# Kernel tuning notes

Measured on AMD Instinct MI355X. Metric: run time of the kernel, lower is better.

Reference implementation:

```python
import math
import jax, jax.numpy as jnp
import numpy as np

B, S, T, C, H = 4, 100, 128, 256, 256
NH, DH = 4, 32            # num_attention_heads//2, hidden_size//num_attention_heads
AH = NH * DH              # all_head_size = 128
FH = 32                   # fire_hidden_size
MAX_SP, MAX_TM, MAX_DOY = 180.0, 365.0, 182.0


def _fire(dist, c, w1, w2, max_dist):
    # FIREDistanceBias: log-compressed distance -> MLP(1->FH, SiLU, FH->1, no bias)
    c = jnp.maximum(c, 0.0)
    d = jnp.log(c * dist + 1.0) / jnp.log(c * max_dist + 1.0)
    h = jax.nn.silu(d[..., None] * w1[:, 0])   # (..., FH)
    return h @ w2[0]                            # (...,)


def setup_inputs() -> dict:
    key = jax.random.key(0)
    ks = jax.random.split(key, 20)
    p = 0.02
    inp = {
        "hidden_states": jax.random.normal(ks[0], (B, S, T, H), jnp.float32),
        "source_embeddings": jax.random.normal(ks[1], (B, S, C, H), jnp.float32),
        "attention_mask": jnp.zeros((B, 1, 1, T, C), jnp.float32),
        "st_dist": jax.random.uniform(ks[2], (B, T, C, 2), jnp.float32)
                   * jnp.array([MAX_SP, MAX_TM], jnp.float32),
        "st_doy_dist": jax.random.uniform(ks[3], (B, T, C), jnp.float32) * MAX_DOY,
        # attention projections (Linear H->AH with bias), output dense (AH->H)
        "Wq": jax.random.normal(ks[4], (AH, H), jnp.float32) * p,
        "bq": jnp.zeros((AH,), jnp.float32),
        "Wk": jax.random.normal(ks[5], (AH, H), jnp.float32) * p,
        "bk": jnp.zeros((AH,), jnp.float32),
        "Wv": jax.random.normal(ks[6], (AH, H), jnp.float32) * p,
        "bv": jnp.zeros((AH,), jnp.float32),
        "Wo": jax.random.normal(ks[7], (H, AH), jnp.float32) * p,
        "bo": jnp.zeros((H,), jnp.float32),
        # FIRE params: spatial / temporal / seasonal
        "c_s": jnp.float32(100.0),
        "w1_s": jax.random.normal(ks[8], (FH, 1), jnp.float32) * 0.5,
        "w2_s": jax.random.normal(ks[9], (1, FH), jnp.float32) * 0.5,
        "c_t": jnp.float32(100.0),
        "w1_t": jax.random.normal(ks[10], (FH, 1), jnp.float32) * 0.5,
        "w2_t": jax.random.normal(ks[11], (1, FH), jnp.float32) * 0.5,
        "c_d": jnp.float32(100.0),
        "w1_d": jax.random.normal(ks[12], (FH, 1), jnp.float32) * 0.5,
        "w2_d": jax.random.normal(ks[13], (1, FH), jnp.float32) * 0.5,
        # per-species log scales (init zeros in torch)
        "s_log_scale": jnp.zeros((S,), jnp.float32),
        "t_log_scale": jnp.zeros((S,), jnp.float32),
    }
    return inp


def reference(hidden_states, source_embeddings, attention_mask, st_dist, st_doy_dist,
              Wq, bq, Wk, bk, Wv, bv, Wo, bo,
              c_s, w1_s, w2_s, c_t, w1_t, w2_t, c_d, w1_d, w2_d,
              s_log_scale, t_log_scale):
    # FIRE distance biases over (B, T, C)
    sb = _fire(st_dist[..., 0], c_s, w1_s, w2_s, MAX_SP)
    tb = _fire(st_dist[..., 1], c_t, w1_t, w2_t, MAX_TM)
    db = _fire(st_doy_dist, c_d, w1_d, w2_d, MAX_DOY)
    # (B, S, T, C): species-scaled spatial+temporal + seasonal bias
    bias = (sb[:, None] * jnp.exp(s_log_scale)[None, :, None, None]
            + tb[:, None] * jnp.exp(t_log_scale)[None, :, None, None]
            + db[:, None])

    # projections; split heads: (B,S,L,AH) -> (B,S,NH,L,DH)
    q = (hidden_states @ Wq.T + bq).reshape(B, S, T, NH, DH).transpose(0, 1, 3, 2, 4)
    k = (source_embeddings @ Wk.T + bk).reshape(B, S, C, NH, DH).transpose(0, 1, 3, 2, 4)
    v = (source_embeddings @ Wv.T + bv).reshape(B, S, C, NH, DH).transpose(0, 1, 3, 2, 4)

    scores = jnp.einsum('bshtd,bshcd->bshtc', q, k) / math.sqrt(DH)
    scores = scores + attention_mask + bias[:, :, None]   # mask (B,1,1,T,C), bias (B,S,1,T,C)
    probs = jax.nn.softmax(scores, axis=-1)
    ctx = jnp.einsum('bshtc,bshcd->bshtd', probs, v)
    ctx = ctx.transpose(0, 1, 3, 2, 4).reshape(B, S, T, AH)
    return ctx @ Wo.T + bo   # STCrossOutput dense (dropout=0, eval)
```

## Files before the change

### kernel.cpp

```cpp
#include <hip/hip_runtime.h>
#include <hip/hip_bf16.h>
#include <math.h>

#define Bdim 4
#define Sdim 100
#define Tdim 128
#define Cdim 256
#define Hdim 256
#define NHd  4
#define DHd  32
#define AHd  128

typedef short bf16x8 __attribute__((ext_vector_type(8)));
typedef float f32x4 __attribute__((ext_vector_type(4)));

#define WAITCNT_V(n) do { \
  asm volatile("s_waitcnt vmcnt(" #n ")" ::: "memory"); \
  __builtin_amdgcn_sched_barrier(0); \
} while (0)

__device__ __forceinline__ short f2b(float x) {
  unsigned u = __float_as_uint(x);
  unsigned r = (u + 0x7FFF + ((u >> 16) & 1)) >> 16;
  return (short)r;
}

__device__ __forceinline__ void split2(float x, short& hi, short& lo) {
  unsigned u = __float_as_uint(x) & 0xFFFF0000u;
  hi = (short)(u >> 16);
  lo = f2b(x - __uint_as_float(u));
}

__device__ __forceinline__ float fire_eval(float dist, float c,
                                           const float* __restrict__ w1,
                                           const float* __restrict__ w2,
                                           float maxd) {
  c = fmaxf(c, 0.0f);
  float d = logf(fmaf(c, dist, 1.0f)) / logf(fmaf(c, maxd, 1.0f));
  float acc = 0.0f;
#pragma unroll
  for (int j = 0; j < 32; ++j) {
    float x = d * w1[j];
    float h = x / (1.0f + expf(-x));
    acc = fmaf(h, w2[j], acc);
  }
  return acc;
}

__global__ __launch_bounds__(256) void fire_bias_kernel(
    const float* __restrict__ st_dist, const float* __restrict__ st_doy,
    const float* __restrict__ mask,
    const float* __restrict__ c_s, const float* __restrict__ w1_s, const float* __restrict__ w2_s,
    const float* __restrict__ c_t, const float* __restrict__ w1_t, const float* __restrict__ w2_t,
    const float* __restrict__ c_d, const float* __restrict__ w1_d, const float* __restrict__ w2_d,
    float* __restrict__ sbF, float* __restrict__ tbF, float* __restrict__ dbF) {
  int i = blockIdx.x * 256 + threadIdx.x;
  if (i >= Bdim * Tdim * Cdim) return;
  int c = i & (Cdim - 1);
  int t = (i >> 8) & (Tdim - 1);
  int b = i >> 15;
  float2 dv = ((const float2*)st_dist)[i];
  float sv = fire_eval(dv.x, c_s[0], w1_s, w2_s, 180.0f);
  float tv = fire_eval(dv.y, c_t[0], w1_t, w2_t, 365.0f);
  float db = fire_eval(st_doy[i], c_d[0], w1_d, w2_d, 182.0f) + mask[i];
  int wt = t >> 4, lg = (t & 15) >> 2, r = t & 3;
  int nt = c >> 4, lr = c & 15;
  size_t off = ((((size_t)(b * 8 + wt) * 16 + nt) * 64) + lg * 16 + lr) * 4 + r;
  sbF[off] = sv;
  tbF[off] = tv;
  dbF[off] = db;
}

__global__ __launch_bounds__(256) void wsplit_pack(
    const float* __restrict__ Wq, const float* __restrict__ Wk,
    const float* __restrict__ Wv, const float* __restrict__ Wo,
    short* __restrict__ pack) {
  int which = blockIdx.y;
  const float* W = which == 0 ? Wq : which == 1 ? Wk : which == 2 ? Wv : Wo;
  int idx = blockIdx.x * 256 + threadIdx.x;
  int j = idx & 7;
  int l = (idx >> 3) & 63;
  int frag = idx >> 9;
  int nt, kk8, Kd;
  if (which == 3) { nt = frag & 15; kk8 = frag >> 4; Kd = 128; }
  else           { nt = frag & 7;  kk8 = frag >> 3; Kd = 256; }
  int n = nt * 16 + (l & 15);
  int k = kk8 * 32 + (l >> 4) * 8 + j;
  float val = W[(size_t)n * Kd + k];
  short h, lo_;
  if (which == 3) split2(val, h, lo_);
  else { h = f2b(val); lo_ = 0; }
  pack[(size_t)which * 65536 + idx] = h;
  pack[(size_t)which * 65536 + 32768 + idx] = lo_;
}

__global__ __launch_bounds__(256, 2) void phase1(
    const float* __restrict__ se,
    const short* __restrict__ Wkp, const float* __restrict__ bk,
    const short* __restrict__ Wvp, const float* __restrict__ bv,
    short* __restrict__ Ko, short* __restrict__ Vo,
    const float* __restrict__ hs, const short* __restrict__ Wqp,
    const float* __restrict__ bq, short* __restrict__ Qb, float scale) {
  __shared__ short wlds[2][16 * 512];
  const int bid = blockIdx.x;
  const int tid = threadIdx.x;
  const int l = tid & 63, w = tid >> 6;
  const int lr = l & 15, lg = l >> 4;
  const int g = bid / 3, m = bid - g * 3;

  if (m < 2) {
    const int m0 = (g * 2 + m) * 128;
    const float* ap0 = se + (size_t)(m0 + w * 32 + lr) * 256 + lg * 8;
    const float* ap1 = ap0 + (size_t)16 * 256;

    auto stage = [&](int buf, int kk) {
#pragma unroll
      for (int r = 0; r < 4; ++r) {
        int f = w + 4 * r;
        const short* gsrc = ((f >> 3) ? Wvp : Wkp) + ((size_t)(kk * 8 + (f & 7)) * 64 + l) * 8;
        int loff = __builtin_amdgcn_readfirstlane(buf * 8192 + f * 512);
        __builtin_amdgcn_global_load_lds(gsrc, &wlds[0][0] + loff, 16, 0, 0);
      }
    };

    f32x4 accK[2][8] = {}, accV[2][8] = {};
    stage(0, 0);
    float4 c0a = *(const float4*)ap0;
    float4 c0b = *(const float4*)(ap0 + 4);
    float4 c1a = *(const float4*)ap1;
    float4 c1b = *(const float4*)(ap1 + 4);
#pragma unroll
    for (int kk = 0; kk < 8; ++kk) {
      const int buf = kk & 1;
      float4 n0a, n0b, n1a, n1b;
      if (kk < 7) {
        stage(buf ^ 1, kk + 1);
        const int nk = (kk + 1) * 32;
        n0a = *(const float4*)(ap0 + nk);
        n0b = *(const float4*)(ap0 + nk + 4);
        n1a = *(const float4*)(ap1 + nk);
        n1b = *(const float4*)(ap1 + nk + 4);
      }
      bf16x8 af[2];
      {
        float a0[8] = {c0a.x, c0a.y, c0a.z, c0a.w, c0b.x, c0b.y, c0b.z, c0b.w};
        float a1[8] = {c1a.x, c1a.y, c1a.z, c1a.w, c1b.x, c1b.y, c1b.z, c1b.w};
#pragma unroll
        for (int e = 0; e < 8; ++e) { af[0][e] = f2b(a0[e]); af[1][e] = f2b(a1[e]); }
      }
      if (kk < 7) { WAITCNT_V(8); } else { WAITCNT_V(0); }
      __builtin_amdgcn_s_barrier();
      const short* lb = &wlds[0][0] + buf * 8192 + l * 8;
#pragma unroll
      for (int nt = 0; nt < 8; ++nt) {
        bf16x8 kw = *(const bf16x8*)(lb + nt * 512);
        bf16x8 vw = *(const bf16x8*)(lb + (8 + nt) * 512);
#pragma unroll
        for (int mi = 0; mi < 2; ++mi) {
          accK[mi][nt] = __builtin_amdgcn_mfma_f32_16x16x32_bf16(af[mi], kw, accK[mi][nt], 0, 0, 0);
          accV[mi][nt] = __builtin_amdgcn_mfma_f32_16x16x32_bf16(af[mi], vw, accV[mi][nt], 0, 0, 0);
        }
      }
      __builtin_amdgcn_s_barrier();
      if (kk < 7) { c0a = n0a; c0b = n0b; c1a = n1a; c1b = n1b; }
    }
#pragma unroll
    for (int mi = 0; mi < 2; ++mi)
#pragma unroll
      for (int nt = 0; nt < 8; ++nt)
#pragma unroll
        for (int r = 0; r < 4; ++r) {
          size_t row = (size_t)(m0 + w * 32 + mi * 16 + lg * 4 + r) * 128 + nt * 16 + lr;
          Ko[row] = f2b(accK[mi][nt][r] + bk[nt * 16 + lr]);
          Vo[row] = f2b(accV[mi][nt][r] + bv[nt * 16 + lr]);
        }
  } else {
    const int m0 = g * 128;
    const float* ap0 = hs + (size_t)(m0 + w * 32 + lr) * 256 + lg * 8;
    const float* ap1 = ap0 + (size_t)16 * 256;

    auto stage = [&](int buf, int kk) {
#pragma unroll
      for (int r = 0; r < 2; ++r) {
        int f = w + 4 * r;
        const short* gsrc = Wqp + ((size_t)(kk * 8 + f) * 64 + l) * 8;
        int loff = __builtin_amdgcn_readfirstlane(buf * 8192 + f * 512);
        __builtin_amdgcn_global_load_lds(gsrc, &wlds[0][0] + loff, 16, 0, 0);
      }
    };

    f32x4 acc[2][8] = {};
    stage(0, 0);
    float4 c0a = *(const float4*)ap0;
    float4 c0b = *(const float4*)(ap0 + 4);
    float4 c1a = *(const float4*)ap1;
    float4 c1b = *(const float4*)(ap1 + 4);
#pragma unroll
    for (int kk = 0; kk < 8; ++kk) {
      const int buf = kk & 1;
      float4 n0a, n0b, n1a, n1b;
      if (kk < 7) {
        stage(buf ^ 1, kk + 1);
        const int nk = (kk + 1) * 32;
        n0a = *(const float4*)(ap0 + nk);
        n0b = *(const float4*)(ap0 + nk + 4);
        n1a = *(const float4*)(ap1 + nk);
        n1b = *(const float4*)(ap1 + nk + 4);
      }
      bf16x8 af[2];
      {
        float a0[8] = {c0a.x, c0a.y, c0a.z, c0a.w, c0b.x, c0b.y, c0b.z, c0b.w};
        float a1[8] = {c1a.x, c1a.y, c1a.z, c1a.w, c1b.x, c1b.y, c1b.z, c1b.w};
#pragma unroll
        for (int e = 0; e < 8; ++e) { af[0][e] = f2b(a0[e]); af[1][e] = f2b(a1[e]); }
      }
      if (kk < 7) { WAITCNT_V(6); } else { WAITCNT_V(0); }
      __builtin_amdgcn_s_barrier();
      const short* lb = &wlds[0][0] + buf * 8192 + l * 8;
#pragma unroll
      for (int nt = 0; nt < 8; ++nt) {
        bf16x8 wv = *(const bf16x8*)(lb + nt * 512);
#pragma unroll
        for (int mi = 0; mi < 2; ++mi)
          acc[mi][nt] = __builtin_amdgcn_mfma_f32_16x16x32_bf16(af[mi], wv, acc[mi][nt], 0, 0, 0);
      }
      __builtin_amdgcn_s_barrier();
      if (kk < 7) { c0a = n0a; c0b = n0b; c1a = n1a; c1b = n1b; }
    }
#pragma unroll
    for (int mi = 0; mi < 2; ++mi)
#pragma unroll
      for (int nt = 0; nt < 8; ++nt)
#pragma unroll
        for (int r = 0; r < 4; ++r)
          Qb[(size_t)(m0 + w * 32 + mi * 16 + lg * 4 + r) * 128 + nt * 16 + lr] =
              f2b((acc[mi][nt][r] + bq[nt * 16 + lr]) * scale);
  }
}

__global__ __launch_bounds__(256, 2) void proj_o_mfma(
    const short* __restrict__ Ahi, const short* __restrict__ Alo,
    const short* __restrict__ Wp, const float* __restrict__ bias,
    float* __restrict__ O) {
  __shared__ short wlds[2][32 * 512];
  const int tid = threadIdx.x;
  const int l = tid & 63, w = tid >> 6;
  const int lr = l & 15, lg = l >> 4;
  const int m0 = blockIdx.x * 128;
  const short* ah0 = Ahi + (size_t)(m0 + w * 32 + lr) * 128 + lg * 8;
  const short* al0 = Alo + (size_t)(m0 + w * 32 + lr) * 128 + lg * 8;
  const short* ah1 = ah0 + (size_t)16 * 128;
  const short* al1 = al0 + (size_t)16 * 128;

  auto stage = [&](int buf, int kk) {
#pragma unroll
    for (int r = 0; r < 8; ++r) {
      int f = w + 4 * r;
      const short* gsrc = Wp + ((f >> 4) ? 32768 : 0)
                          + ((size_t)(kk * 16 + (f & 15)) * 64 + l) * 8;
      int loff = __builtin_amdgcn_readfirstlane(buf * 16384 + f * 512);
      __builtin_amdgcn_global_load_lds(gsrc, &wlds[0][0] + loff, 16, 0, 0);
    }
  };

  f32x4 acc[2][16] = {};
  stage(0, 0);
  bf16x8 ch0 = *(const bf16x8*)ah0;
  bf16x8 cl0 = *(const bf16x8*)al0;
  bf16x8 ch1 = *(const bf16x8*)ah1;
  bf16x8 cl1 = *(const bf16x8*)al1;
#pragma unroll
  for (int kk = 0; kk < 4; ++kk) {
    const int buf = kk & 1;
    bf16x8 nh0, nl0, nh1, nl1;
    if (kk < 3) {
      stage(buf ^ 1, kk + 1);
      const int nk = (kk + 1) * 32;
      nh0 = *(const bf16x8*)(ah0 + nk);
      nl0 = *(const bf16x8*)(al0 + nk);
      nh1 = *(const bf16x8*)(ah1 + nk);
      nl1 = *(const bf16x8*)(al1 + nk);
    }
    if (kk < 3) { WAITCNT_V(12); } else { WAITCNT_V(0); }
    __builtin_amdgcn_s_barrier();
    bf16x8 ahi[2] = {ch0, ch1};
    bf16x8 alo[2] = {cl0, cl1};
    const short* lb = &wlds[0][0] + buf * 16384 + l * 8;
#pragma unroll
    for (int nt = 0; nt < 16; ++nt) {
      bf16x8 whi = *(const bf16x8*)(lb + nt * 512);
      bf16x8 wlo = *(const bf16x8*)(lb + (16 + nt) * 512);
#pragma unroll
      for (int mi = 0; mi < 2; ++mi) {
        acc[mi][nt] = __builtin_amdgcn_mfma_f32_16x16x32_bf16(ahi[mi], whi, acc[mi][nt], 0, 0, 0);
        acc[mi][nt] = __builtin_amdgcn_mfma_f32_16x16x32_bf16(ahi[mi], wlo, acc[mi][nt], 0, 0, 0);
        acc[mi][nt] = __builtin_amdgcn_mfma_f32_16x16x32_bf16(alo[mi], whi, acc[mi][nt], 0, 0, 0);
      }
    }
    __builtin_amdgcn_s_barrier();
    if (kk < 3) { ch0 = nh0; cl0 = nl0; ch1 = nh1; cl1 = nl1; }
  }
#pragma unroll
  for (int mi = 0; mi < 2; ++mi)
#pragma unroll
    for (int nt = 0; nt < 16; ++nt)
#pragma unroll
      for (int r = 0; r < 4; ++r)
        O[(size_t)(m0 + w * 32 + mi * 16 + lg * 4 + r) * 256 + nt * 16 + lr] =
            acc[mi][nt][r] + bias[nt * 16 + lr];
}

__global__ __launch_bounds__(512, 2) void attn_mfma(
    const short* __restrict__ Qb, const short* __restrict__ Kb,
    const short* __restrict__ Vb,
    const float* __restrict__ sbF, const float* __restrict__ tbF,
    const float* __restrict__ dbF,
    const float* __restrict__ sls, const float* __restrict__ tls,
    short* __restrict__ Chi, short* __restrict__ Clo) {
  __shared__ short vfrag[8][2][64][8];
  __shared__ short pbuf[8][16 * 36];

  const int tid = threadIdx.x;
  const int l = tid & 63;
  const int w = tid >> 6;
  const int lr = l & 15, lg = l >> 4;
  const int bid = blockIdx.x;
  const int xcd = bid & 7;
  const int i_  = bid >> 3;
  const int bs  = xcd * 50 + (i_ >> 2);
  const int h   = i_ & 3;
  const int s = bs % Sdim, b = bs / Sdim;
  const float es = __expf(sls[s]);
  const float et = __expf(tls[s]);

  const size_t kvbase = (size_t)bs * Cdim * AHd + h * DHd;
  const size_t qbase  = (size_t)bs * Tdim * AHd + h * DHd;

  bf16x8 qf = *(const bf16x8*)(Qb + qbase + (size_t)(w * 16 + lr) * AHd + lg * 8);
  bf16x8 kf[16];
#pragma unroll
  for (int nt = 0; nt < 16; ++nt)
    kf[nt] = *(const bf16x8*)(Kb + kvbase + (size_t)(nt * 16 + lr) * AHd + lg * 8);

#pragma unroll
  for (int rep = 0; rep < 2; ++rep) {
    int chunk = tid * 2 + rep;
    int c = chunk >> 2, q = chunk & 3;
    bf16x8 v8 = *(const bf16x8*)(Vb + kvbase + (size_t)c * AHd + q * 8);
    int kc = c >> 5, nt = q >> 1;
    int lanebase = ((c & 31) >> 3) * 16 + (q & 1) * 8;
    int j = c & 7;
#pragma unroll
    for (int e = 0; e < 8; ++e) {
      int row = lanebase + e;
      int prow = row ^ ((row >> 4) << 1);
      vfrag[kc][nt][prow][j] = v8[e];
    }
  }
  __syncthreads();

  const size_t bfrag = ((size_t)(b * 8 + w) * 16) * 64 + l;
  const float4* sb4 = (const float4*)sbF + bfrag;
  const float4* tb4 = (const float4*)tbF + bfrag;
  const float4* db4 = (const float4*)dbF + bfrag;
  f32x4 sacc[16];
#pragma unroll
  for (int nt = 0; nt < 16; ++nt) {
    float4 sv = sb4[nt * 64];
    float4 tv = tb4[nt * 64];
    float4 dv = db4[nt * 64];
    f32x4 cinit;
    cinit[0] = fmaf(sv.x, es, fmaf(tv.x, et, dv.x));
    cinit[1] = fmaf(sv.y, es, fmaf(tv.y, et, dv.y));
    cinit[2] = fmaf(sv.z, es, fmaf(tv.z, et, dv.z));
    cinit[3] = fmaf(sv.w, es, fmaf(tv.w, et, dv.w));
    sacc[nt] = __builtin_amdgcn_mfma_f32_16x16x32_bf16(qf, kf[nt], cinit, 0, 0, 0);
  }

  float rinv[4];
#pragma unroll
  for (int nt = 0; nt < 16; ++nt)
#pragma unroll
    for (int r = 0; r < 4; ++r)
      sacc[nt][r] = __expf(sacc[nt][r]);
#pragma unroll
  for (int r = 0; r < 4; ++r) {
    float su = 0.f;
#pragma unroll
    for (int nt = 0; nt < 16; ++nt) su += sacc[nt][r];
#pragma unroll
    for (int off = 1; off < 16; off <<= 1) su += __shfl_xor(su, off);
    rinv[r] = 1.0f / su;
  }

  const f32x4 zero = {0.f, 0.f, 0.f, 0.f};
  f32x4 cacc[2] = {zero, zero};
  short* pb = &pbuf[w][0];
  const int lp = l ^ ((l >> 4) << 1);
#pragma unroll
  for (int kc = 0; kc < 8; ++kc) {
#pragma unroll
    for (int ntl = 0; ntl < 2; ++ntl) {
      int nt = kc * 2 + ntl;
#pragma unroll
      for (int r = 0; r < 4; ++r)
        pb[(lg * 4 + r) * 36 + ntl * 16 + lr] = f2b(sacc[nt][r]);
    }
    bf16x8 af = *(const bf16x8*)&pb[lr * 36 + lg * 8];
#pragma unroll
    for (int ntd = 0; ntd < 2; ++ntd) {
      bf16x8 vf = *(const bf16x8*)&vfrag[kc][ntd][lp][0];
      cacc[ntd] = __builtin_amdgcn_mfma_f32_16x16x32_bf16(af, vf, cacc[ntd], 0, 0, 0);
    }
  }

#pragma unroll
  for (int ntd = 0; ntd < 2; ++ntd)
#pragma unroll
    for (int r = 0; r < 4; ++r) {
      float val = cacc[ntd][r] * rinv[r];
      short h_, lo_;
      split2(val, h_, lo_);
      size_t idx = qbase + (size_t)(w * 16 + lg * 4 + r) * AHd + ntd * 16 + lr;
      Chi[idx] = h_;
      Clo[idx] = lo_;
    }
}

extern "C" void kernel_launch(void* const* d_in, const int* in_sizes, int n_in,
                              void* d_out, int out_size, void* d_ws, size_t ws_size,
                              hipStream_t stream) {
  const float* hs     = (const float*)d_in[0];
  const float* se     = (const float*)d_in[1];
  const float* mask   = (const float*)d_in[2];
  const float* stdist = (const float*)d_in[3];
  const float* stdoy  = (const float*)d_in[4];
  const float* Wq = (const float*)d_in[5];
  const float* bq = (const float*)d_in[6];
  const float* Wk = (const float*)d_in[7];
  const float* bk = (const float*)d_in[8];
  const float* Wv = (const float*)d_in[9];
  const float* bv = (const float*)d_in[10];
  const float* Wo = (const float*)d_in[11];
  const float* bo = (const float*)d_in[12];
  const float* c_s  = (const float*)d_in[13];
  const float* w1_s = (const float*)d_in[14];
  const float* w2_s = (const float*)d_in[15];
  const float* c_t  = (const float*)d_in[16];
  const float* w1_t = (const float*)d_in[17];
  const float* w2_t = (const float*)d_in[18];
  const float* c_d  = (const float*)d_in[19];
  const float* w1_d = (const float*)d_in[20];
  const float* w2_d = (const float*)d_in[21];
  const float* sls  = (const float*)d_in[22];
  const float* tls  = (const float*)d_in[23];
  float* out = (float*)d_out;

  float* ws = (float*)d_ws;
  const size_t BTC  = (size_t)Bdim * Tdim * Cdim;
  const size_t NQ   = (size_t)Bdim * Sdim * Tdim * AHd;
  const size_t NKV  = (size_t)Bdim * Sdim * Cdim * AHd;

  float* sbF  = ws;
  float* tbF  = sbF + BTC;
  float* dbF  = tbF + BTC;
  short* wpck = (short*)(dbF + BTC);
  short* Qb   = wpck + 262144;
  short* Kb   = Qb + NQ;
  short* Vb   = Kb + NKV;
  short* Chi  = Vb + NKV;
  short* Clo  = Chi + NQ;

  const int MQ  = Bdim * Sdim * Tdim;

  fire_bias_kernel<<<(Bdim * Tdim * Cdim + 255) / 256, 256, 0, stream>>>(
      stdist, stdoy, mask, c_s, w1_s, w2_s, c_t, w1_t, w2_t, c_d, w1_d, w2_d,
      sbF, tbF, dbF);

  wsplit_pack<<<dim3(128, 4), 256, 0, stream>>>(Wq, Wk, Wv, Wo, wpck);

  phase1<<<dim3(1200), 256, 0, stream>>>(
      se, wpck + 65536, bk, wpck + 131072, bv, Kb, Vb,
      hs, wpck, bq, Qb, 0.17677669529663687f);

  attn_mfma<<<dim3(Bdim * Sdim * NHd), 512, 0, stream>>>(
      Qb, Kb, Vb, sbF, tbF, dbF, sls, tls, Chi, Clo);

  proj_o_mfma<<<dim3(MQ / 128), 256, 0, stream>>>(Chi, Clo, wpck + 196608, bo, out);
}
```

Before: 164.5 us.

## Fuse QKV projection, attention and output projection into one kernel per (b,s)

Replaces the separate phase1 (Q/K/V projection), attn_mfma and proj_o_mfma kernels with a single fused kernel that handles one (batch, species) pair per 512-thread block. K and V are computed into LDS fragments, Q is projected per wave directly from global weights, attention runs over all four heads in turn, and the output dense layer is applied in registers. The intent is to stop writing Q/K/V and the split context tensors to global memory and reading them back. In exchange the grid shrinks to 400 blocks with large LDS use, which can lower occupancy and parallelism, and the Wq and Wo weights are read straight from global memory rather than staged through LDS.

```diff
diff --git a/kernel.cpp b/kernel.cpp
--- a/kernel.cpp
+++ b/kernel.cpp
@@ -18,6 +18,8 @@
   asm volatile("s_waitcnt vmcnt(" #n ")" ::: "memory"); \
   __builtin_amdgcn_sched_barrier(0); \
 } while (0)
+
+#define MFMA16(a, b, c) __builtin_amdgcn_mfma_f32_16x16x32_bf16((a), (b), (c), 0, 0, 0)
 
 __device__ __forceinline__ short f2b(float x) {
   unsigned u = __float_as_uint(x);
@@ -94,41 +96,52 @@
   pack[(size_t)which * 65536 + 32768 + idx] = lo_;
 }
 
-__global__ __launch_bounds__(256, 2) void phase1(
-    const float* __restrict__ se,
-    const short* __restrict__ Wkp, const float* __restrict__ bk,
-    const short* __restrict__ Wvp, const float* __restrict__ bv,
-    short* __restrict__ Ko, short* __restrict__ Vo,
-    const float* __restrict__ hs, const short* __restrict__ Wqp,
-    const float* __restrict__ bq, short* __restrict__ Qb, float scale) {
-  __shared__ short wlds[2][16 * 512];
-  const int bid = blockIdx.x;
+__global__ __launch_bounds__(512, 2) void fused_attn(
+    const float* __restrict__ hs, const float* __restrict__ se,
+    const short* __restrict__ Wqp, const short* __restrict__ Wkp,
+    const short* __restrict__ Wvp, const short* __restrict__ Wop,
+    const float* __restrict__ bq, const float* __restrict__ bk,
+    const float* __restrict__ bv, const float* __restrict__ bo,
+    const float* __restrict__ sbF, const float* __restrict__ tbF,
+    const float* __restrict__ dbF,
+    const float* __restrict__ sls, const float* __restrict__ tls,
+    float* __restrict__ out) {
+  __shared__ short kfs[4][16][64][8];
+  __shared__ short vfs[8][8][64][8];
+  __shared__ short wst[16384];
+
   const int tid = threadIdx.x;
   const int l = tid & 63, w = tid >> 6;
   const int lr = l & 15, lg = l >> 4;
-  const int g = bid / 3, m = bid - g * 3;
-
-  if (m < 2) {
-    const int m0 = (g * 2 + m) * 128;
-    const float* ap0 = se + (size_t)(m0 + w * 32 + lr) * 256 + lg * 8;
+  const int bid = blockIdx.x;
+  const int bs = (bid & 7) * 50 + (bid >> 3);
+  const int s = bs % Sdim, b = bs / Sdim;
+  const float es = __expf(sls[s]), et = __expf(tls[s]);
+
+  float bkv[8], bvv[8], bqv[8];
+#pragma unroll
+  for (int nt = 0; nt < 8; ++nt) {
+    bkv[nt] = bk[nt * 16 + lr];
+    bvv[nt] = bv[nt * 16 + lr];
+    bqv[nt] = bq[nt * 16 + lr];
+  }
+
+  {
+    const int cw0 = w * 32;
+    const float* ap0 = se + ((size_t)bs * 256 + cw0 + lr) * 256 + lg * 8;
     const float* ap1 = ap0 + (size_t)16 * 256;
-
     auto stage = [&](int buf, int kk) {
 #pragma unroll
-      for (int r = 0; r < 4; ++r) {
-        int f = w + 4 * r;
-        const short* gsrc = ((f >> 3) ? Wvp : Wkp) + ((size_t)(kk * 8 + (f & 7)) * 64 + l) * 8;
-        int loff = __builtin_amdgcn_readfirstlane(buf * 8192 + f * 512);
-        __builtin_amdgcn_global_load_lds(gsrc, &wlds[0][0] + loff, 16, 0, 0);
+      for (int r = 0; r < 2; ++r) {
+        const short* gsrc = (r ? Wvp : Wkp) + ((size_t)(kk * 8 + w) * 64 + l) * 8;
+        int loff = __builtin_amdgcn_readfirstlane(buf * 8192 + (w + 8 * r) * 512);
+        __builtin_amdgcn_global_load_lds(gsrc, &wst[0] + loff, 16, 0, 0);
       }
     };
-
     f32x4 accK[2][8] = {}, accV[2][8] = {};
     stage(0, 0);
-    float4 c0a = *(const float4*)ap0;
-    float4 c0b = *(const float4*)(ap0 + 4);
-    float4 c1a = *(const float4*)ap1;
-    float4 c1b = *(const float4*)(ap1 + 4);
+    float4 c0a = *(const float4*)ap0, c0b = *(const float4*)(ap0 + 4);
+    float4 c1a = *(const float4*)ap1, c1b = *(const float4*)(ap1 + 4);
 #pragma unroll
     for (int kk = 0; kk < 8; ++kk) {
       const int buf = kk & 1;
@@ -136,10 +149,8 @@
       if (kk < 7) {
         stage(buf ^ 1, kk + 1);
         const int nk = (kk + 1) * 32;
-        n0a = *(const float4*)(ap0 + nk);
-        n0b = *(const float4*)(ap0 + nk + 4);
-        n1a = *(const float4*)(ap1 + nk);
-        n1b = *(const float4*)(ap1 + nk + 4);
+        n0a = *(const float4*)(ap0 + nk); n0b = *(const float4*)(ap0 + nk + 4);
+        n1a = *(const float4*)(ap1 + nk); n1b = *(const float4*)(ap1 + nk + 4);
       }
       bf16x8 af[2];
       {
@@ -148,17 +159,17 @@
 #pragma unroll
         for (int e = 0; e < 8; ++e) { af[0][e] = f2b(a0[e]); af[1][e] = f2b(a1[e]); }
       }
-      if (kk < 7) { WAITCNT_V(8); } else { WAITCNT_V(0); }
+      if (kk < 7) { WAITCNT_V(6); } else { WAITCNT_V(0); }
       __builtin_amdgcn_s_barrier();
-      const short* lb = &wlds[0][0] + buf * 8192 + l * 8;
+      const short* lb = &wst[0] + buf * 8192 + l * 8;
 #pragma unroll
       for (int nt = 0; nt < 8; ++nt) {
         bf16x8 kw = *(const bf16x8*)(lb + nt * 512);
         bf16x8 vw = *(const bf16x8*)(lb + (8 + nt) * 512);
 #pragma unroll
         for (int mi = 0; mi < 2; ++mi) {
-          accK[mi][nt] = __builtin_amdgcn_mfma_f32_16x16x32_bf16(af[mi], kw, accK[mi][nt], 0, 0, 0);
-          accV[mi][nt] = __builtin_amdgcn_mfma_f32_16x16x32_bf16(af[mi], vw, accV[mi][nt], 0, 0, 0);
+          accK[mi][nt] = MFMA16(af[mi], kw, accK[mi][nt]);
+          accV[mi][nt] = MFMA16(af[mi], vw, accV[mi][nt]);
         }
       }
       __builtin_amdgcn_s_barrier();
@@ -170,261 +181,147 @@
       for (int nt = 0; nt < 8; ++nt)
 #pragma unroll
         for (int r = 0; r < 4; ++r) {
-          size_t row = (size_t)(m0 + w * 32 + mi * 16 + lg * 4 + r) * 128 + nt * 16 + lr;
-          Ko[row] = f2b(accK[mi][nt][r] + bk[nt * 16 + lr]);
-          Vo[row] = f2b(accV[mi][nt][r] + bv[nt * 16 + lr]);
+          kfs[nt >> 1][w * 2 + mi][((nt & 1) * 2 + (lr >> 3)) * 16 + lg * 4 + r][lr & 7] =
+              f2b(accK[mi][nt][r] + bkv[nt]);
+          vfs[w][nt][(mi * 2 + (lg >> 1)) * 16 + lr][(lg & 1) * 4 + r] =
+              f2b(accV[mi][nt][r] + bvv[nt]);
         }
-  } else {
-    const int m0 = g * 128;
-    const float* ap0 = hs + (size_t)(m0 + w * 32 + lr) * 256 + lg * 8;
-    const float* ap1 = ap0 + (size_t)16 * 256;
-
-    auto stage = [&](int buf, int kk) {
-#pragma unroll
-      for (int r = 0; r < 2; ++r) {
-        int f = w + 4 * r;
-        const short* gsrc = Wqp + ((size_t)(kk * 8 + f) * 64 + l) * 8;
-        int loff = __builtin_amdgcn_readfirstlane(buf * 8192 + f * 512);
-        __builtin_amdgcn_global_load_lds(gsrc, &wlds[0][0] + loff, 16, 0, 0);
-      }
-    };
-
-    f32x4 acc[2][8] = {};
-    stage(0, 0);
-    float4 c0a = *(const float4*)ap0;
-    float4 c0b = *(const float4*)(ap0 + 4);
-    float4 c1a = *(const float4*)ap1;
-    float4 c1b = *(const float4*)(ap1 + 4);
+  }
+  __syncthreads();
+
+  f32x4 qacc[8] = {};
+  {
+    const float* qp = hs + ((size_t)bs * 128 + w * 16 + lr) * 256 + lg * 8;
+    float4 qa = *(const float4*)qp, qb2 = *(const float4*)(qp + 4);
 #pragma unroll
     for (int kk = 0; kk < 8; ++kk) {
-      const int buf = kk & 1;
-      float4 n0a, n0b, n1a, n1b;
+      float4 na, nb;
       if (kk < 7) {
-        stage(buf ^ 1, kk + 1);
-        const int nk = (kk + 1) * 32;
-        n0a = *(const float4*)(ap0 + nk);
-        n0b = *(const float4*)(ap0 + nk + 4);
-        n1a = *(const float4*)(ap1 + nk);
-        n1b = *(const float4*)(ap1 + nk + 4);
-      }
-      bf16x8 af[2];
+        na = *(const float4*)(qp + (kk + 1) * 32);
+        nb = *(const float4*)(qp + (kk + 1) * 32 + 4);
+      }
+      bf16x8 af;
       {
-        float a0[8] = {c0a.x, c0a.y, c0a.z, c0a.w, c0b.x, c0b.y, c0b.z, c0b.w};
-        float a1[8] = {c1a.x, c1a.y, c1a.z, c1a.w, c1b.x, c1b.y, c1b.z, c1b.w};
-#pragma unroll
-        for (int e = 0; e < 8; ++e) { af[0][e] = f2b(a0[e]); af[1][e] = f2b(a1[e]); }
-      }
-      if (kk < 7) { WAITCNT_V(6); } else { WAITCNT_V(0); }
-      __builtin_amdgcn_s_barrier();
-      const short* lb = &wlds[0][0] + buf * 8192 + l * 8;
+        float a0[8] = {qa.x, qa.y, qa.z, qa.w, qb2.x, qb2.y, qb2.z, qb2.w};
+#pragma unroll
+        for (int e = 0; e < 8; ++e) af[e] = f2b(a0[e]);
+      }
 #pragma unroll
       for (int nt = 0; nt < 8; ++nt) {
-        bf16x8 wv = *(const bf16x8*)(lb + nt * 512);
-#pragma unroll
-        for (int mi = 0; mi < 2; ++mi)
-          acc[mi][nt] = __builtin_amdgcn_mfma_f32_16x16x32_bf16(af[mi], wv, acc[mi][nt], 0, 0, 0);
-      }
-      __builtin_amdgcn_s_barrier();
-      if (kk < 7) { c0a = n0a; c0b = n0b; c1a = n1a; c1b = n1b; }
-    }
-#pragma unroll
-    for (int mi = 0; mi < 2; ++mi)
-#pragma unroll
-      for (int nt = 0; nt < 8; ++nt)
-#pragma unroll
-        for (int r = 0; r < 4; ++r)
-          Qb[(size_t)(m0 + w * 32 + mi * 16 + lg * 4 + r) * 128 + nt * 16 + lr] =
-              f2b((acc[mi][nt][r] + bq[nt * 16 + lr]) * scale);
-  }
-}
-
-__global__ __launch_bounds__(256, 2) void proj_o_mfma(
-    const short* __restrict__ Ahi, const short* __restrict__ Alo,
-    const short* __restrict__ Wp, const float* __restrict__ bias,
-    float* __restrict__ O) {
-  __shared__ short wlds[2][32 * 512];
-  const int tid = threadIdx.x;
-  const int l = tid & 63, w = tid >> 6;
-  const int lr = l & 15, lg = l >> 4;
-  const int m0 = blockIdx.x * 128;
-  const short* ah0 = Ahi + (size_t)(m0 + w * 32 + lr) * 128 + lg * 8;
-  const short* al0 = Alo + (size_t)(m0 + w * 32 + lr) * 128 + lg * 8;
-  const short* ah1 = ah0 + (size_t)16 * 128;
-  const short* al1 = al0 + (size_t)16 * 128;
-
-  auto stage = [&](int buf, int kk) {
-#pragma unroll
-    for (int r = 0; r < 8; ++r) {
-      int f = w + 4 * r;
-      const short* gsrc = Wp + ((f >> 4) ? 32768 : 0)
-                          + ((size_t)(kk * 16 + (f & 15)) * 64 + l) * 8;
-      int loff = __builtin_amdgcn_readfirstlane(buf * 16384 + f * 512);
-      __builtin_amdgcn_global_load_lds(gsrc, &wlds[0][0] + loff, 16, 0, 0);
-    }
-  };
-
-  f32x4 acc[2][16] = {};
-  stage(0, 0);
-  bf16x8 ch0 = *(const bf16x8*)ah0;
-  bf16x8 cl0 = *(const bf16x8*)al0;
-  bf16x8 ch1 = *(const bf16x8*)ah1;
-  bf16x8 cl1 = *(const bf16x8*)al1;
-#pragma unroll
-  for (int kk = 0; kk < 4; ++kk) {
-    const int buf = kk & 1;
-    bf16x8 nh0, nl0, nh1, nl1;
-    if (kk < 3) {
-      stage(buf ^ 1, kk + 1);
-      const int nk = (kk + 1) * 32;
-      nh0 = *(const bf16x8*)(ah0 + nk);
-      nl0 = *(const bf16x8*)(al0 + nk);
-      nh1 = *(const bf16x8*)(ah1 + nk);
-      nl1 = *(const bf16x8*)(al1 + nk);
-    }
-    if (kk < 3) { WAITCNT_V(12); } else { WAITCNT_V(0); }
-    __builtin_amdgcn_s_barrier();
-    bf16x8 ahi[2] = {ch0, ch1};
-    bf16x8 alo[2] = {cl0, cl1};
-    const short* lb = &wlds[0][0] + buf * 16384 + l * 8;
-#pragma unroll
-    for (int nt = 0; nt < 16; ++nt) {
-      bf16x8 whi = *(const bf16x8*)(lb + nt * 512);
-      bf16x8 wlo = *(const bf16x8*)(lb + (16 + nt) * 512);
-#pragma unroll
-      for (int mi = 0; mi < 2; ++mi) {
-        acc[mi][nt] = __builtin_amdgcn_mfma_f32_16x16x32_bf16(ahi[mi], whi, acc[mi][nt], 0, 0, 0);
-        acc[mi][nt] = __builtin_amdgcn_mfma_f32_16x16x32_bf16(ahi[mi], wlo, acc[mi][nt], 0, 0, 0);
-        acc[mi][nt] = __builtin_amdgcn_mfma_f32_16x16x32_bf16(alo[mi], whi, acc[mi][nt], 0, 0, 0);
-      }
-    }
-    __builtin_amdgcn_s_barrier();
-    if (kk < 3) { ch0 = nh0; cl0 = nl0; ch1 = nh1; cl1 = nl1; }
-  }
-#pragma unroll
-  for (int mi = 0; mi < 2; ++mi)
-#pragma unroll
-    for (int nt = 0; nt < 16; ++nt)
-#pragma unroll
-      for (int r = 0; r < 4; ++r)
-        O[(size_t)(m0 + w * 32 + mi * 16 + lg * 4 + r) * 256 + nt * 16 + lr] =
-            acc[mi][nt][r] + bias[nt * 16 + lr];
-}
-
-__global__ __launch_bounds__(512, 2) void attn_mfma(
-    const short* __restrict__ Qb, const short* __restrict__ Kb,
-    const short* __restrict__ Vb,
-    const float* __restrict__ sbF, const float* __restrict__ tbF,
-    const float* __restrict__ dbF,
-    const float* __restrict__ sls, const float* __restrict__ tls,
-    short* __restrict__ Chi, short* __restrict__ Clo) {
-  __shared__ short vfrag[8][2][64][8];
-  __shared__ short pbuf[8][16 * 36];
-
-  const int tid = threadIdx.x;
-  const int l = tid & 63;
-  const int w = tid >> 6;
-  const int lr = l & 15, lg = l >> 4;
-  const int bid = blockIdx.x;
-  const int xcd = bid & 7;
-  const int i_  = bid >> 3;
-  const int bs  = xcd * 50 + (i_ >> 2);
-  const int h   = i_ & 3;
-  const int s = bs % Sdim, b = bs / Sdim;
-  const float es = __expf(sls[s]);
-  const float et = __expf(tls[s]);
-
-  const size_t kvbase = (size_t)bs * Cdim * AHd + h * DHd;
-  const size_t qbase  = (size_t)bs * Tdim * AHd + h * DHd;
-
-  bf16x8 qf = *(const bf16x8*)(Qb + qbase + (size_t)(w * 16 + lr) * AHd + lg * 8);
-  bf16x8 kf[16];
-#pragma unroll
-  for (int nt = 0; nt < 16; ++nt)
-    kf[nt] = *(const bf16x8*)(Kb + kvbase + (size_t)(nt * 16 + lr) * AHd + lg * 8);
-
-#pragma unroll
-  for (int rep = 0; rep < 2; ++rep) {
-    int chunk = tid * 2 + rep;
-    int c = chunk >> 2, q = chunk & 3;
-    bf16x8 v8 = *(const bf16x8*)(Vb + kvbase + (size_t)c * AHd + q * 8);
-    int kc = c >> 5, nt = q >> 1;
-    int lanebase = ((c & 31) >> 3) * 16 + (q & 1) * 8;
-    int j = c & 7;
-#pragma unroll
-    for (int e = 0; e < 8; ++e) {
-      int row = lanebase + e;
-      int prow = row ^ ((row >> 4) << 1);
-      vfrag[kc][nt][prow][j] = v8[e];
-    }
-  }
-  __syncthreads();
-
+        bf16x8 wv = *(const bf16x8*)(Wqp + ((size_t)(kk * 8 + nt) * 64 + l) * 8);
+        qacc[nt] = MFMA16(af, wv, qacc[nt]);
+      }
+      if (kk < 7) { qa = na; qb2 = nb; }
+    }
+  }
+
+  short* pb = &wst[0] + w * 2048;
+  const float sc = 0.17677669529663687f;
   const size_t bfrag = ((size_t)(b * 8 + w) * 16) * 64 + l;
   const float4* sb4 = (const float4*)sbF + bfrag;
   const float4* tb4 = (const float4*)tbF + bfrag;
   const float4* db4 = (const float4*)dbF + bfrag;
-  f32x4 sacc[16];
-#pragma unroll
-  for (int nt = 0; nt < 16; ++nt) {
-    float4 sv = sb4[nt * 64];
-    float4 tv = tb4[nt * 64];
-    float4 dv = db4[nt * 64];
-    f32x4 cinit;
-    cinit[0] = fmaf(sv.x, es, fmaf(tv.x, et, dv.x));
-    cinit[1] = fmaf(sv.y, es, fmaf(tv.y, et, dv.y));
-    cinit[2] = fmaf(sv.z, es, fmaf(tv.z, et, dv.z));
-    cinit[3] = fmaf(sv.w, es, fmaf(tv.w, et, dv.w));
-    sacc[nt] = __builtin_amdgcn_mfma_f32_16x16x32_bf16(qf, kf[nt], cinit, 0, 0, 0);
-  }
-
-  float rinv[4];
+  const f32x4 zero = {0.f, 0.f, 0.f, 0.f};
+  f32x4 cacc[4][2];
+
+#pragma unroll
+  for (int h = 0; h < 4; ++h) {
+#pragma unroll
+    for (int ntl = 0; ntl < 2; ++ntl) {
+      const int ntq = h * 2 + ntl;
+#pragma unroll
+      for (int r = 0; r < 4; ++r)
+        pb[(lg * 4 + r) * 36 + ntl * 16 + lr] = f2b((qacc[ntq][r] + bqv[ntq]) * sc);
+    }
+    bf16x8 qf = *(const bf16x8*)&pb[lr * 36 + lg * 8];
+
+    f32x4 sacc[16];
+#pragma unroll
+    for (int ntc = 0; ntc < 16; ++ntc) {
+      bf16x8 kf = *(const bf16x8*)&kfs[h][ntc][l][0];
+      float4 sv = sb4[ntc * 64];
+      float4 tv = tb4[ntc * 64];
+      float4 dv = db4[ntc * 64];
+      f32x4 ci;
+      ci[0] = fmaf(sv.x, es, fmaf(tv.x, et, dv.x));
+      ci[1] = fmaf(sv.y, es, fmaf(tv.y, et, dv.y));
+      ci[2] = fmaf(sv.z, es, fmaf(tv.z, et, dv.z));
+      ci[3] = fmaf(sv.w, es, fmaf(tv.w, et, dv.w));
+      sacc[ntc] = MFMA16(qf, kf, ci);
+    }
+
+    float rinv[4];
+#pragma unroll
+    for (int nt = 0; nt < 16; ++nt)
+#pragma unroll
+      for (int r = 0; r < 4; ++r)
+        sacc[nt][r] = __expf(sacc[nt][r]);
+#pragma unroll
+    for (int r = 0; r < 4; ++r) {
+      float su = 0.f;
+#pragma unroll
+      for (int nt = 0; nt < 16; ++nt) su += sacc[nt][r];
+#pragma unroll
+      for (int off = 1; off < 16; off <<= 1) su += __shfl_xor(su, off);
+      rinv[r] = 1.0f / su;
+    }
+
+    cacc[h][0] = zero; cacc[h][1] = zero;
+#pragma unroll
+    for (int kc = 0; kc < 8; ++kc) {
+#pragma unroll
+      for (int ntl = 0; ntl < 2; ++ntl) {
+        const int nt = kc * 2 + ntl;
+#pragma unroll
+        for (int r = 0; r < 4; ++r)
+          pb[(lg * 4 + r) * 36 + ntl * 16 + lr] = f2b(sacc[nt][r]);
+      }
+      bf16x8 af = *(const bf16x8*)&pb[lr * 36 + lg * 8];
+#pragma unroll
+      for (int ntd = 0; ntd < 2; ++ntd) {
+        bf16x8 vf = *(const bf16x8*)&vfs[kc][h * 2 + ntd][l][0];
+        cacc[h][ntd] = MFMA16(af, vf, cacc[h][ntd]);
+      }
+    }
+#pragma unroll
+    for (int ntd = 0; ntd < 2; ++ntd)
+#pragma unroll
+      for (int r = 0; r < 4; ++r)
+        cacc[h][ntd][r] *= rinv[r];
+  }
+
+  short* phi = pb;
+  short* plo = pb + 576;
+  f32x4 oacc[16] = {};
+#pragma unroll
+  for (int kk = 0; kk < 4; ++kk) {
+#pragma unroll
+    for (int ntd = 0; ntd < 2; ++ntd)
+#pragma unroll
+      for (int r = 0; r < 4; ++r) {
+        short h_, lo_;
+        split2(cacc[kk][ntd][r], h_, lo_);
+        phi[(lg * 4 + r) * 36 + ntd * 16 + lr] = h_;
+        plo[(lg * 4 + r) * 36 + ntd * 16 + lr] = lo_;
+      }
+    bf16x8 ahi = *(const bf16x8*)&phi[lr * 36 + lg * 8];
+    bf16x8 alo = *(const bf16x8*)&plo[lr * 36 + lg * 8];
+#pragma unroll
+    for (int nt = 0; nt < 16; ++nt) {
+      size_t wof = ((size_t)(kk * 16 + nt) * 64 + l) * 8;
+      bf16x8 whi = *(const bf16x8*)(Wop + wof);
+      bf16x8 wlo = *(const bf16x8*)(Wop + 32768 + wof);
+      oacc[nt] = MFMA16(ahi, whi, oacc[nt]);
+      oacc[nt] = MFMA16(ahi, wlo, oacc[nt]);
+      oacc[nt] = MFMA16(alo, whi, oacc[nt]);
+    }
+  }
 #pragma unroll
   for (int nt = 0; nt < 16; ++nt)
 #pragma unroll
     for (int r = 0; r < 4; ++r)
-      sacc[nt][r] = __expf(sacc[nt][r]);
-#pragma unroll
-  for (int r = 0; r < 4; ++r) {
-    float su = 0.f;
-#pragma unroll
-    for (int nt = 0; nt < 16; ++nt) su += sacc[nt][r];
-#pragma unroll
-    for (int off = 1; off < 16; off <<= 1) su += __shfl_xor(su, off);
-    rinv[r] = 1.0f / su;
-  }
-
-  const f32x4 zero = {0.f, 0.f, 0.f, 0.f};
-  f32x4 cacc[2] = {zero, zero};
-  short* pb = &pbuf[w][0];
-  const int lp = l ^ ((l >> 4) << 1);
-#pragma unroll
-  for (int kc = 0; kc < 8; ++kc) {
-#pragma unroll
-    for (int ntl = 0; ntl < 2; ++ntl) {
-      int nt = kc * 2 + ntl;
-#pragma unroll
-      for (int r = 0; r < 4; ++r)
-        pb[(lg * 4 + r) * 36 + ntl * 16 + lr] = f2b(sacc[nt][r]);
-    }
-    bf16x8 af = *(const bf16x8*)&pb[lr * 36 + lg * 8];
-#pragma unroll
-    for (int ntd = 0; ntd < 2; ++ntd) {
-      bf16x8 vf = *(const bf16x8*)&vfrag[kc][ntd][lp][0];
-      cacc[ntd] = __builtin_amdgcn_mfma_f32_16x16x32_bf16(af, vf, cacc[ntd], 0, 0, 0);
-    }
-  }
-
-#pragma unroll
-  for (int ntd = 0; ntd < 2; ++ntd)
-#pragma unroll
-    for (int r = 0; r < 4; ++r) {
-      float val = cacc[ntd][r] * rinv[r];
-      short h_, lo_;
-      split2(val, h_, lo_);
-      size_t idx = qbase + (size_t)(w * 16 + lg * 4 + r) * AHd + ntd * 16 + lr;
-      Chi[idx] = h_;
-      Clo[idx] = lo_;
-    }
+      out[((size_t)bs * 128 + w * 16 + lg * 4 + r) * 256 + nt * 16 + lr] =
+          oacc[nt][r] + bo[nt * 16 + lr];
 }
 
 extern "C" void kernel_launch(void* const* d_in, const int* in_sizes, int n_in,
@@ -457,21 +354,12 @@
   float* out = (float*)d_out;
 
   float* ws = (float*)d_ws;
-  const size_t BTC  = (size_t)Bdim * Tdim * Cdim;
-  const size_t NQ   = (size_t)Bdim * Sdim * Tdim * AHd;
-  const size_t NKV  = (size_t)Bdim * Sdim * Cdim * AHd;
+  const size_t BTC = (size_t)Bdim * Tdim * Cdim;
 
   float* sbF  = ws;
   float* tbF  = sbF + BTC;
   float* dbF  = tbF + BTC;
   short* wpck = (short*)(dbF + BTC);
-  short* Qb   = wpck + 262144;
-  short* Kb   = Qb + NQ;
-  short* Vb   = Kb + NKV;
-  short* Chi  = Vb + NKV;
-  short* Clo  = Chi + NQ;
-
-  const int MQ  = Bdim * Sdim * Tdim;
 
   fire_bias_kernel<<<(Bdim * Tdim * Cdim + 255) / 256, 256, 0, stream>>>(
       stdist, stdoy, mask, c_s, w1_s, w2_s, c_t, w1_t, w2_t, c_d, w1_d, w2_d,
@@ -479,12 +367,9 @@
 
   wsplit_pack<<<dim3(128, 4), 256, 0, stream>>>(Wq, Wk, Wv, Wo, wpck);
 
-  phase1<<<dim3(1200), 256, 0, stream>>>(
-      se, wpck + 65536, bk, wpck + 131072, bv, Kb, Vb,
-      hs, wpck, bq, Qb, 0.17677669529663687f);
-
-  attn_mfma<<<dim3(Bdim * Sdim * NHd), 512, 0, stream>>>(
-      Qb, Kb, Vb, sbF, tbF, dbF, sls, tls, Chi, Clo);
-
-  proj_o_mfma<<<dim3(MQ / 128), 256, 0, stream>>>(Chi, Clo, wpck + 196608, bo, out);
-}
+  fused_attn<<<dim3(Bdim * Sdim), 512, 0, stream>>>(
+      hs, se,
+      wpck, wpck + 65536, wpck + 131072, wpck + 196608,
+      bq, bk, bv, bo,
+      sbF, tbF, dbF, sls, tls, out);
+}
```

New measurement: 234.9 us. 42.8% more time.
